# Kernel optimization log

Measured on AMD Instinct MI355X. Metric: run time of the kernel, lower is better.

## Reference

```python
import jax, jax.numpy as jnp
import numpy as np

N = 512
D_OBJ = 256
D_BOX = 128
D_IN = 2 * D_OBJ + D_BOX  # 640 = sum(input_dim)
HID = 256
D_OUT = 256               # sum(output_dim)
BN_EPS = 1e-5


def setup_inputs() -> dict:
    key = jax.random.key(0)
    ks = jax.random.split(key, 16)
    sc = lambda d: 1.0 / np.sqrt(d)
    inp = {
        "object_feats": jax.random.normal(ks[0], (N, D_OBJ), jnp.float32),
        "bboxes_embedding": jax.random.normal(ks[1], (N, N, D_BOX), jnp.float32),
        "mask": (jax.random.uniform(ks[2], (N, N)) > 0.3).astype(jnp.float32),
        # weight_mlp: Linear(D_IN->HID), LeakyReLU, BatchNorm1d(HID) [eval], Dropout [eval], Linear(HID->1)
        "w1": jax.random.normal(ks[3], (HID, D_IN), jnp.float32) * sc(D_IN),
        "b1": jnp.zeros((HID,), jnp.float32),
        "bn_gamma": jnp.ones((HID,), jnp.float32),
        "bn_beta": jnp.zeros((HID,), jnp.float32),
        "bn_mean": jnp.zeros((HID,), jnp.float32),
        "bn_var": jnp.ones((HID,), jnp.float32),
        "w2": jax.random.normal(ks[4], (1, HID), jnp.float32) * sc(HID),
        "b2": jnp.zeros((1,), jnp.float32),
        # conv: Linear(D_IN->HID), ReLU, Linear(HID->D_OUT)
        "cw1": jax.random.normal(ks[5], (HID, D_IN), jnp.float32) * sc(D_IN),
        "cb1": jnp.zeros((HID,), jnp.float32),
        "cw2": jax.random.normal(ks[6], (D_OUT, HID), jnp.float32) * sc(HID),
        "cb2": jnp.zeros((D_OUT,), jnp.float32),
    }
    return inp


def reference(object_feats, bboxes_embedding, mask, w1, b1, bn_gamma, bn_beta,
              bn_mean, bn_var, w2, b2, cw1, cb1, cw2, cb2):
    n = object_feats.shape[0]
    d = object_feats.shape[1]
    # all N^2 pairs (i, j) in row-major order: concat(feat_i, feat_j, bbox_ij)
    feats = jnp.concatenate([
        jnp.broadcast_to(object_feats[:, None, :], (n, n, d)),
        jnp.broadcast_to(object_feats[None, :, :], (n, n, d)),
        bboxes_embedding,
    ], axis=-1)                                        # [N, N, D_IN]

    # weight_mlp -> per-pair confidence scalar
    h = feats @ w1.T + b1                              # [N, N, HID]
    h = jnp.where(h > 0, h, 0.01 * h)                  # LeakyReLU(0.01)
    h = (h - bn_mean) * jax.lax.rsqrt(bn_var + BN_EPS) * bn_gamma + bn_beta
    conf = (h @ w2.T + b2)[..., 0]                     # [N, N]

    # row-wise softmax over j, masked renormalization
    conf = jax.nn.softmax(conf, axis=-1)
    conf = conf * mask
    conf = conf / (jnp.sum(conf, axis=-1, keepdims=True) + 1e-8)

    # conv MLP per pair, then weighted-sum reduce over neighbors j
    g = jax.nn.relu(feats @ cw1.T + cb1)               # [N, N, HID]
    out = g @ cw2.T + cb2                              # [N, N, D_OUT]
    new_feats = jnp.einsum('ij,ijd->id', conf, out)    # [N, D_OUT]
    return new_feats
```

## Files before the change

### kernel.cpp

```cpp
#include <hip/hip_runtime.h>
#include <hip/hip_bf16.h>

#define NN   512
#define DOBJ 256
#define DBOX 128
#define DIN  640
#define HID  256
#define DOUT 256

typedef __attribute__((ext_vector_type(8))) short  short8;
typedef __attribute__((ext_vector_type(4))) float  f32x4;

#define OFF_A    0u
#define OFF_B    131072u
#define OFF_CA   262144u
#define OFF_CB   393216u
#define OFF_WSV  524288u
#define OFF_S    524544u
#define OFF_CONF 525312u
#define OFF_G    787456u
#define OFF_WSWZ 918528u

__device__ __forceinline__ ushort bf16u(float x) {
    __hip_bfloat16 h = __float2bfloat16(x);
    union { __hip_bfloat16 b; ushort u; } c; c.b = h;
    return c.u;
}

__device__ __forceinline__ short8 cvt8(float4 a, float4 b) {
    short8 o;
    o[0] = (short)bf16u(a.x); o[1] = (short)bf16u(a.y);
    o[2] = (short)bf16u(a.z); o[3] = (short)bf16u(a.w);
    o[4] = (short)bf16u(b.x); o[5] = (short)bf16u(b.y);
    o[6] = (short)bf16u(b.z); o[7] = (short)bf16u(b.w);
    return o;
}

__global__ __launch_bounds__(256, 2) void k_pre_mfma(
    const float* __restrict__ obj, const float* __restrict__ w1,
    const float* __restrict__ cw1, const float* __restrict__ b1,
    const float* __restrict__ cb1,
    float* __restrict__ A, float* __restrict__ B,
    float* __restrict__ Ca, float* __restrict__ Cb)
{
    const int bx = blockIdx.x;
    const int i0 = blockIdx.y * 64;
    const int tid = threadIdx.x;
    const int w = tid >> 6, lane = tid & 63;
    const int lr = lane & 15, lg = lane >> 4;

    const float* src = (bx & 2) ? cw1 : w1;
    const int dof = (bx & 1) * DOBJ;

    f32x4 acc[4][4];
#pragma unroll
    for (int a = 0; a < 4; ++a)
#pragma unroll
        for (int b = 0; b < 4; ++b) acc[a][b] = (f32x4){0.f, 0.f, 0.f, 0.f};

#pragma unroll
    for (int ks = 0; ks < 8; ++ks) {
        short8 af[4], bf[4];
#pragma unroll
        for (int ms = 0; ms < 4; ++ms) {
            const float* ap = obj + (size_t)(i0 + ms * 16 + lr) * DOBJ + ks * 32 + lg * 8;
            af[ms] = cvt8(*(const float4*)ap, *(const float4*)(ap + 4));
        }
#pragma unroll
        for (int t = 0; t < 4; ++t) {
            const int kc = w * 64 + t * 16 + lr;
            const float* bp = src + (size_t)kc * DIN + dof + ks * 32 + lg * 8;
            bf[t] = cvt8(*(const float4*)bp, *(const float4*)(bp + 4));
        }
#pragma unroll
        for (int ms = 0; ms < 4; ++ms)
#pragma unroll
            for (int t = 0; t < 4; ++t)
                acc[ms][t] = __builtin_amdgcn_mfma_f32_16x16x32_bf16(
                    af[ms], bf[t], acc[ms][t], 0, 0, 0);
    }

    float* dst = (bx == 0) ? A : (bx == 1) ? B : (bx == 2) ? Ca : Cb;
    const float* bias = (bx == 0) ? b1 : (bx == 2) ? cb1 : nullptr;
    float bb[4];
#pragma unroll
    for (int t = 0; t < 4; ++t)
        bb[t] = bias ? bias[w * 64 + t * 16 + lr] : 0.f;

#pragma unroll
    for (int ms = 0; ms < 4; ++ms)
#pragma unroll
        for (int t = 0; t < 4; ++t)
#pragma unroll
            for (int r = 0; r < 4; ++r) {
                const int i = i0 + ms * 16 + lg * 4 + r;
                const int kc = w * 64 + t * 16 + lr;
                dst[(size_t)i * HID + kc] = acc[ms][t][r] + bb[t];
            }
}

__global__ void k_wsvec(const float* __restrict__ w2, const float* __restrict__ gamma,
                        const float* __restrict__ var, float* __restrict__ wsv)
{
    const int k = threadIdx.x;
    wsv[k] = w2[k] * gamma[k] * rsqrtf(var[k] + 1e-5f);
}

__global__ __launch_bounds__(128) void k_wprep(
    const float* __restrict__ w1, const float* __restrict__ cw1,
    ushort* __restrict__ wswz)
{
    const int k = blockIdx.x, mat = blockIdx.y, d = threadIdx.x;
    const float* src = mat ? cw1 : w1;
    const float v = src[(size_t)k * DIN + 2 * DOBJ + d];
    const int c = d >> 3;
    const int idx = k * 128 + (((c ^ (k & 7)) << 3)) + (d & 7);
    wswz[(size_t)mat * 32768 + idx] = bf16u(v);
}

template<int GACC>
__global__ __launch_bounds__(256, 2) void k_pair(
    const float* __restrict__ bbox, const ushort* __restrict__ wswz,
    const float* __restrict__ Arow,
    const float* __restrict__ Bcol,
    const float* __restrict__ aux,
    float* __restrict__ outp)
{
    const int i  = blockIdx.y;
    const int j0 = blockIdx.x * 64;
    const int tid = threadIdx.x;
    const int w = tid >> 6, lane = tid & 63;
    const int lr = lane & 15, lg = lane >> 4;

    __shared__ ushort wlds[32768];
    __shared__ float  red[4][64];
    __shared__ float  conf_s[64];

    {
        const uint4* g = (const uint4*)wswz;
        uint4* l = (uint4*)wlds;
#pragma unroll
        for (int n = 0; n < 16; ++n) l[n * 256 + tid] = g[n * 256 + tid];
    }
    if (GACC && tid < 64) conf_s[tid] = aux[(size_t)i * NN + j0 + tid];
    __syncthreads();

    float as_t[4], ws_t[4];
#pragma unroll
    for (int t = 0; t < 4; ++t) {
        const int kk = w * 64 + t * 16 + lr;
        as_t[t] = Arow[(size_t)i * HID + kk];
        ws_t[t] = GACC ? 0.f : aux[kk];
    }

    f32x4 acc[4][4];
#pragma unroll
    for (int a = 0; a < 4; ++a)
#pragma unroll
        for (int b = 0; b < 4; ++b) acc[a][b] = (f32x4){0.f, 0.f, 0.f, 0.f};

#pragma unroll
    for (int ks = 0; ks < 4; ++ks) {
        short8 bf[4];
#pragma unroll
        for (int t = 0; t < 4; ++t) {
            const int kk = w * 64 + t * 16 + lr;
            const int c  = (ks * 4 + lg) ^ (lr & 7);
            bf[t] = *(const short8*)&wlds[kk * 128 + (c << 3)];
        }
#pragma unroll
        for (int ms = 0; ms < 4; ++ms) {
            const float* ap = bbox +
                (((size_t)i * NN + j0 + ms * 16 + lr) * DBOX + ks * 32 + lg * 8);
            const float4 a0 = *(const float4*)ap;
            const float4 a1 = *(const float4*)(ap + 4);
            const short8 af = cvt8(a0, a1);
#pragma unroll
            for (int t = 0; t < 4; ++t)
                acc[ms][t] = __builtin_amdgcn_mfma_f32_16x16x32_bf16(
                    af, bf[t], acc[ms][t], 0, 0, 0);
        }
    }

    if (!GACC) {
        float pj[4][4];
#pragma unroll
        for (int a = 0; a < 4; ++a)
#pragma unroll
            for (int b = 0; b < 4; ++b) pj[a][b] = 0.f;
#pragma unroll
        for (int ms = 0; ms < 4; ++ms)
#pragma unroll
            for (int r = 0; r < 4; ++r) {
                const int j = j0 + ms * 16 + lg * 4 + r;
                const float* Bj = Bcol + (size_t)j * HID + w * 64 + lr;
#pragma unroll
                for (int t = 0; t < 4; ++t) {
                    float h = acc[ms][t][r] + as_t[t] + Bj[t * 16];
                    h = fmaxf(h, 0.01f * h);
                    pj[ms][r] = fmaf(h, ws_t[t], pj[ms][r]);
                }
            }
#pragma unroll
        for (int ms = 0; ms < 4; ++ms)
#pragma unroll
            for (int r = 0; r < 4; ++r) {
                float v = pj[ms][r];
                v += __shfl_xor(v, 1);  v += __shfl_xor(v, 2);
                v += __shfl_xor(v, 4);  v += __shfl_xor(v, 8);
                if (lr == 0) red[w][ms * 16 + lg * 4 + r] = v;
            }
        __syncthreads();
        if (tid < 64)
            outp[(size_t)i * NN + j0 + tid] =
                red[0][tid] + red[1][tid] + red[2][tid] + red[3][tid];
    } else {
        float cf[4][4];
#pragma unroll
        for (int ms = 0; ms < 4; ++ms)
#pragma unroll
            for (int r = 0; r < 4; ++r) cf[ms][r] = conf_s[ms * 16 + lg * 4 + r];
        float gk[4] = {0.f, 0.f, 0.f, 0.f};
#pragma unroll
        for (int ms = 0; ms < 4; ++ms)
#pragma unroll
            for (int r = 0; r < 4; ++r) {
                const int j = j0 + ms * 16 + lg * 4 + r;
                const float* Bj = Bcol + (size_t)j * HID + w * 64 + lr;
#pragma unroll
                for (int t = 0; t < 4; ++t) {
                    float h = acc[ms][t][r] + as_t[t] + Bj[t * 16];
                    h = fmaxf(h, 0.f);
                    gk[t] = fmaf(cf[ms][r], h, gk[t]);
                }
            }
#pragma unroll
        for (int t = 0; t < 4; ++t) {
            float v = gk[t];
            v += __shfl_xor(v, 16);
            v += __shfl_xor(v, 32);
            if (lg == 0)
                atomicAdd(&outp[(size_t)i * DOUT + w * 64 + t * 16 + lr], v);
        }
    }
}

__global__ __launch_bounds__(256) void k_softmax(
    const float* __restrict__ conf_raw, const float* __restrict__ mask,
    float* __restrict__ conf, float* __restrict__ s_out)
{
    const int i = blockIdx.x, tid = threadIdx.x;
    const int lane = tid & 63, w = tid >> 6;
    __shared__ float wred[3][4];

    const float r0 = conf_raw[(size_t)i * NN + tid];
    const float r1 = conf_raw[(size_t)i * NN + 256 + tid];
    const float mk0 = mask[(size_t)i * NN + tid];
    const float mk1 = mask[(size_t)i * NN + 256 + tid];

    float m = fmaxf(r0, r1);
#pragma unroll
    for (int off = 32; off; off >>= 1) m = fmaxf(m, __shfl_down(m, off));
    if (lane == 0) wred[0][w] = m;
    __syncthreads();
    const float M = fmaxf(fmaxf(wred[0][0], wred[0][1]), fmaxf(wred[0][2], wred[0][3]));

    const float e0 = __expf(r0 - M), e1 = __expf(r1 - M);
    float sa = e0 + e1;
    float sk = e0 * mk0 + e1 * mk1;
#pragma unroll
    for (int off = 32; off; off >>= 1) {
        sa += __shfl_down(sa, off);
        sk += __shfl_down(sk, off);
    }
    if (lane == 0) { wred[1][w] = sa; wred[2][w] = sk; }
    __syncthreads();
    const float SA = wred[1][0] + wred[1][1] + wred[1][2] + wred[1][3];
    const float SK = wred[2][0] + wred[2][1] + wred[2][2] + wred[2][3];
    const float dinv = 1.f / (SK + 1e-8f * SA);

    conf[(size_t)i * NN + tid]       = e0 * mk0 * dinv;
    conf[(size_t)i * NN + 256 + tid] = e1 * mk1 * dinv;
    if (tid == 0) s_out[i] = SK * dinv;
}

__global__ __launch_bounds__(256) void k_out(
    const float* __restrict__ G, const float* __restrict__ cw2,
    const float* __restrict__ cb2, const float* __restrict__ s_in,
    float* __restrict__ out)
{
    const int i = blockIdx.x, o = threadIdx.x;
    __shared__ float Gs[DOUT];
    Gs[o] = G[(size_t)i * DOUT + o];
    __syncthreads();
    const float* wr = cw2 + (size_t)o * HID;
    float acc = 0.f;
#pragma unroll 4
    for (int k = 0; k < HID; ++k) acc = fmaf(Gs[k], wr[k], acc);
    out[(size_t)i * DOUT + o] = acc + s_in[i] * cb2[o];
}

extern "C" void kernel_launch(void* const* d_in, const int* in_sizes, int n_in,
                              void* d_out, int out_size, void* d_ws, size_t ws_size,
                              hipStream_t stream)
{
    const float* obj  = (const float*)d_in[0];
    const float* bbox = (const float*)d_in[1];
    const float* mask = (const float*)d_in[2];
    const float* w1   = (const float*)d_in[3];
    const float* b1   = (const float*)d_in[4];
    const float* bn_g = (const float*)d_in[5];
    const float* bn_v = (const float*)d_in[8];
    const float* w2   = (const float*)d_in[9];
    const float* cw1  = (const float*)d_in[11];
    const float* cb1  = (const float*)d_in[12];
    const float* cw2  = (const float*)d_in[13];
    const float* cb2  = (const float*)d_in[14];

    float* ws   = (float*)d_ws;
    float* A    = ws + OFF_A;
    float* B    = ws + OFF_B;
    float* Ca   = ws + OFF_CA;
    float* Cb   = ws + OFF_CB;
    float* wsv  = ws + OFF_WSV;
    float* sbuf = ws + OFF_S;
    float* conf = ws + OFF_CONF;
    float* G    = ws + OFF_G;
    ushort* wswz = (ushort*)(ws + OFF_WSWZ);
    float* out  = (float*)d_out;

    k_pre_mfma<<<dim3(4, 8), 256, 0, stream>>>(obj, w1, cw1, b1, cb1, A, B, Ca, Cb);
    k_wsvec<<<1, 256, 0, stream>>>(w2, bn_g, bn_v, wsv);
    k_wprep<<<dim3(256, 2), 128, 0, stream>>>(w1, cw1, wswz);
    k_pair<0><<<dim3(8, NN), 256, 0, stream>>>(bbox, wswz, A, B, wsv, conf);
    k_softmax<<<NN, 256, 0, stream>>>(conf, mask, conf, sbuf);
    hipMemsetAsync(G, 0, (size_t)NN * DOUT * sizeof(float), stream);
    k_pair<1><<<dim3(8, NN), 256, 0, stream>>>(bbox, wswz + 32768, Ca, Cb, conf, G);
    k_out<<<NN, 256, 0, stream>>>(G, cw2, cb2, sbuf, out);
}
```

Measured before the change: 451.4 us.

## Fuse softmax into conf pair kernel and make G accumulation row-local

Restructures both pair kernels so one 512-thread block handles a whole row i, looping over four 128-column chunks. The row-wise softmax and mask renormalization are fused into the confidence kernel, and the G accumulation is reduced in shared memory instead of with global atomics. This removes the separate softmax launch, the memset, and the atomic traffic, and loads the LDS weights once per row instead of once per 64 columns. The cost is only 512 blocks with a serial j loop per block, which may lower parallelism and latency hiding.

```diff
diff --git a/kernel.cpp b/kernel.cpp
--- a/kernel.cpp
+++ b/kernel.cpp
@@ -118,170 +118,203 @@
     wswz[(size_t)mat * 32768 + idx] = bf16u(v);
 }
 
-template<int GACC>
-__global__ __launch_bounds__(256, 2) void k_pair(
+__global__ __launch_bounds__(512, 4) void k_conf_fused(
     const float* __restrict__ bbox, const ushort* __restrict__ wswz,
-    const float* __restrict__ Arow,
-    const float* __restrict__ Bcol,
-    const float* __restrict__ aux,
-    float* __restrict__ outp)
-{
-    const int i  = blockIdx.y;
-    const int j0 = blockIdx.x * 64;
+    const float* __restrict__ A_, const float* __restrict__ B_,
+    const float* __restrict__ wsv, const float* __restrict__ mask,
+    float* __restrict__ conf, float* __restrict__ s_out)
+{
+    const int i = blockIdx.x;
     const int tid = threadIdx.x;
-    const int w = tid >> 6, lane = tid & 63;
+    const int wv = tid >> 6, lane = tid & 63;
+    const int jw = wv >> 2, kw = wv & 3;
     const int lr = lane & 15, lg = lane >> 4;
 
     __shared__ ushort wlds[32768];
-    __shared__ float  red[4][64];
-    __shared__ float  conf_s[64];
+    __shared__ float  red[4][512];
+    __shared__ float  wred[3][8];
 
     {
         const uint4* g = (const uint4*)wswz;
         uint4* l = (uint4*)wlds;
 #pragma unroll
-        for (int n = 0; n < 16; ++n) l[n * 256 + tid] = g[n * 256 + tid];
-    }
-    if (GACC && tid < 64) conf_s[tid] = aux[(size_t)i * NN + j0 + tid];
+        for (int n = 0; n < 8; ++n) l[n * 512 + tid] = g[n * 512 + tid];
+    }
     __syncthreads();
 
     float as_t[4], ws_t[4];
 #pragma unroll
     for (int t = 0; t < 4; ++t) {
-        const int kk = w * 64 + t * 16 + lr;
-        as_t[t] = Arow[(size_t)i * HID + kk];
-        ws_t[t] = GACC ? 0.f : aux[kk];
-    }
-
-    f32x4 acc[4][4];
-#pragma unroll
-    for (int a = 0; a < 4; ++a)
-#pragma unroll
-        for (int b = 0; b < 4; ++b) acc[a][b] = (f32x4){0.f, 0.f, 0.f, 0.f};
-
-#pragma unroll
-    for (int ks = 0; ks < 4; ++ks) {
-        short8 bf[4];
-#pragma unroll
-        for (int t = 0; t < 4; ++t) {
-            const int kk = w * 64 + t * 16 + lr;
-            const int c  = (ks * 4 + lg) ^ (lr & 7);
-            bf[t] = *(const short8*)&wlds[kk * 128 + (c << 3)];
+        const int kk = kw * 64 + t * 16 + lr;
+        as_t[t] = A_[(size_t)i * HID + kk];
+        ws_t[t] = wsv[kk];
+    }
+
+    for (int it = 0; it < 4; ++it) {
+        const int j0 = it * 128 + jw * 64;
+
+        f32x4 acc[4][4];
+#pragma unroll
+        for (int a = 0; a < 4; ++a)
+#pragma unroll
+            for (int b = 0; b < 4; ++b) acc[a][b] = (f32x4){0.f, 0.f, 0.f, 0.f};
+
+#pragma unroll
+        for (int ks = 0; ks < 4; ++ks) {
+            short8 bf[4];
+#pragma unroll
+            for (int t = 0; t < 4; ++t) {
+                const int kk = kw * 64 + t * 16 + lr;
+                const int c  = (ks * 4 + lg) ^ (lr & 7);
+                bf[t] = *(const short8*)&wlds[kk * 128 + (c << 3)];
+            }
+#pragma unroll
+            for (int ms = 0; ms < 4; ++ms) {
+                const float* ap = bbox +
+                    (((size_t)i * NN + j0 + ms * 16 + lr) * DBOX + ks * 32 + lg * 8);
+                const short8 af = cvt8(*(const float4*)ap, *(const float4*)(ap + 4));
+#pragma unroll
+                for (int t = 0; t < 4; ++t)
+                    acc[ms][t] = __builtin_amdgcn_mfma_f32_16x16x32_bf16(
+                        af, bf[t], acc[ms][t], 0, 0, 0);
+            }
         }
-#pragma unroll
-        for (int ms = 0; ms < 4; ++ms) {
-            const float* ap = bbox +
-                (((size_t)i * NN + j0 + ms * 16 + lr) * DBOX + ks * 32 + lg * 8);
-            const float4 a0 = *(const float4*)ap;
-            const float4 a1 = *(const float4*)(ap + 4);
-            const short8 af = cvt8(a0, a1);
-#pragma unroll
-            for (int t = 0; t < 4; ++t)
-                acc[ms][t] = __builtin_amdgcn_mfma_f32_16x16x32_bf16(
-                    af, bf[t], acc[ms][t], 0, 0, 0);
-        }
-    }
-
-    if (!GACC) {
-        float pj[4][4];
-#pragma unroll
-        for (int a = 0; a < 4; ++a)
-#pragma unroll
-            for (int b = 0; b < 4; ++b) pj[a][b] = 0.f;
+
 #pragma unroll
         for (int ms = 0; ms < 4; ++ms)
 #pragma unroll
             for (int r = 0; r < 4; ++r) {
                 const int j = j0 + ms * 16 + lg * 4 + r;
-                const float* Bj = Bcol + (size_t)j * HID + w * 64 + lr;
+                const float* Bj = B_ + (size_t)j * HID + kw * 64 + lr;
+                float pj = 0.f;
 #pragma unroll
                 for (int t = 0; t < 4; ++t) {
                     float h = acc[ms][t][r] + as_t[t] + Bj[t * 16];
                     h = fmaxf(h, 0.01f * h);
-                    pj[ms][r] = fmaf(h, ws_t[t], pj[ms][r]);
+                    pj = fmaf(h, ws_t[t], pj);
                 }
-            }
-#pragma unroll
-        for (int ms = 0; ms < 4; ++ms)
-#pragma unroll
-            for (int r = 0; r < 4; ++r) {
-                float v = pj[ms][r];
-                v += __shfl_xor(v, 1);  v += __shfl_xor(v, 2);
-                v += __shfl_xor(v, 4);  v += __shfl_xor(v, 8);
-                if (lr == 0) red[w][ms * 16 + lg * 4 + r] = v;
-            }
-        __syncthreads();
-        if (tid < 64)
-            outp[(size_t)i * NN + j0 + tid] =
-                red[0][tid] + red[1][tid] + red[2][tid] + red[3][tid];
-    } else {
-        float cf[4][4];
-#pragma unroll
-        for (int ms = 0; ms < 4; ++ms)
-#pragma unroll
-            for (int r = 0; r < 4; ++r) cf[ms][r] = conf_s[ms * 16 + lg * 4 + r];
-        float gk[4] = {0.f, 0.f, 0.f, 0.f};
+                pj += __shfl_xor(pj, 1);  pj += __shfl_xor(pj, 2);
+                pj += __shfl_xor(pj, 4);  pj += __shfl_xor(pj, 8);
+                if (lr == 0) red[kw][j] = pj;
+            }
+    }
+    __syncthreads();
+
+    const float r0 = red[0][tid] + red[1][tid] + red[2][tid] + red[3][tid];
+    const float mk = mask[(size_t)i * NN + tid];
+
+    float m = r0;
+#pragma unroll
+    for (int off = 32; off; off >>= 1) m = fmaxf(m, __shfl_xor(m, off));
+    if (lane == 0) wred[0][wv] = m;
+    __syncthreads();
+    float M = wred[0][0];
+#pragma unroll
+    for (int u = 1; u < 8; ++u) M = fmaxf(M, wred[0][u]);
+
+    const float e = __expf(r0 - M);
+    float sa = e, sk = e * mk;
+#pragma unroll
+    for (int off = 32; off; off >>= 1) {
+        sa += __shfl_xor(sa, off);
+        sk += __shfl_xor(sk, off);
+    }
+    if (lane == 0) { wred[1][wv] = sa; wred[2][wv] = sk; }
+    __syncthreads();
+    float SA = 0.f, SK = 0.f;
+#pragma unroll
+    for (int u = 0; u < 8; ++u) { SA += wred[1][u]; SK += wred[2][u]; }
+    const float dinv = 1.f / (SK + 1e-8f * SA);
+
+    conf[(size_t)i * NN + tid] = e * mk * dinv;
+    if (tid == 0) s_out[i] = SK * dinv;
+}
+
+__global__ __launch_bounds__(512, 4) void k_gacc_fused(
+    const float* __restrict__ bbox, const ushort* __restrict__ wswz,
+    const float* __restrict__ Ca_, const float* __restrict__ Cb_,
+    const float* __restrict__ conf, float* __restrict__ G)
+{
+    const int i = blockIdx.x;
+    const int tid = threadIdx.x;
+    const int wv = tid >> 6, lane = tid & 63;
+    const int jw = wv >> 2, kw = wv & 3;
+    const int lr = lane & 15, lg = lane >> 4;
+
+    __shared__ ushort wlds[32768];
+    __shared__ float  conf_s[512];
+    __shared__ float  gred[2][256];
+
+    {
+        const uint4* g = (const uint4*)wswz;
+        uint4* l = (uint4*)wlds;
+#pragma unroll
+        for (int n = 0; n < 8; ++n) l[n * 512 + tid] = g[n * 512 + tid];
+    }
+    conf_s[tid] = conf[(size_t)i * NN + tid];
+    __syncthreads();
+
+    float as_t[4];
+#pragma unroll
+    for (int t = 0; t < 4; ++t)
+        as_t[t] = Ca_[(size_t)i * HID + kw * 64 + t * 16 + lr];
+
+    float gk[4] = {0.f, 0.f, 0.f, 0.f};
+
+    for (int it = 0; it < 4; ++it) {
+        const int j0 = it * 128 + jw * 64;
+
+        f32x4 acc[4][4];
+#pragma unroll
+        for (int a = 0; a < 4; ++a)
+#pragma unroll
+            for (int b = 0; b < 4; ++b) acc[a][b] = (f32x4){0.f, 0.f, 0.f, 0.f};
+
+#pragma unroll
+        for (int ks = 0; ks < 4; ++ks) {
+            short8 bf[4];
+#pragma unroll
+            for (int t = 0; t < 4; ++t) {
+                const int kk = kw * 64 + t * 16 + lr;
+                const int c  = (ks * 4 + lg) ^ (lr & 7);
+                bf[t] = *(const short8*)&wlds[kk * 128 + (c << 3)];
+            }
+#pragma unroll
+            for (int ms = 0; ms < 4; ++ms) {
+                const float* ap = bbox +
+                    (((size_t)i * NN + j0 + ms * 16 + lr) * DBOX + ks * 32 + lg * 8);
+                const short8 af = cvt8(*(const float4*)ap, *(const float4*)(ap + 4));
+#pragma unroll
+                for (int t = 0; t < 4; ++t)
+                    acc[ms][t] = __builtin_amdgcn_mfma_f32_16x16x32_bf16(
+                        af, bf[t], acc[ms][t], 0, 0, 0);
+            }
+        }
+
 #pragma unroll
         for (int ms = 0; ms < 4; ++ms)
 #pragma unroll
             for (int r = 0; r < 4; ++r) {
                 const int j = j0 + ms * 16 + lg * 4 + r;
-                const float* Bj = Bcol + (size_t)j * HID + w * 64 + lr;
+                const float cf = conf_s[j];
+                const float* Bj = Cb_ + (size_t)j * HID + kw * 64 + lr;
 #pragma unroll
                 for (int t = 0; t < 4; ++t) {
                     float h = acc[ms][t][r] + as_t[t] + Bj[t * 16];
-                    h = fmaxf(h, 0.f);
-                    gk[t] = fmaf(cf[ms][r], h, gk[t]);
+                    gk[t] = fmaf(cf, fmaxf(h, 0.f), gk[t]);
                 }
             }
-#pragma unroll
-        for (int t = 0; t < 4; ++t) {
-            float v = gk[t];
-            v += __shfl_xor(v, 16);
-            v += __shfl_xor(v, 32);
-            if (lg == 0)
-                atomicAdd(&outp[(size_t)i * DOUT + w * 64 + t * 16 + lr], v);
-        }
-    }
-}
-
-__global__ __launch_bounds__(256) void k_softmax(
-    const float* __restrict__ conf_raw, const float* __restrict__ mask,
-    float* __restrict__ conf, float* __restrict__ s_out)
-{
-    const int i = blockIdx.x, tid = threadIdx.x;
-    const int lane = tid & 63, w = tid >> 6;
-    __shared__ float wred[3][4];
-
-    const float r0 = conf_raw[(size_t)i * NN + tid];
-    const float r1 = conf_raw[(size_t)i * NN + 256 + tid];
-    const float mk0 = mask[(size_t)i * NN + tid];
-    const float mk1 = mask[(size_t)i * NN + 256 + tid];
-
-    float m = fmaxf(r0, r1);
-#pragma unroll
-    for (int off = 32; off; off >>= 1) m = fmaxf(m, __shfl_down(m, off));
-    if (lane == 0) wred[0][w] = m;
-    __syncthreads();
-    const float M = fmaxf(fmaxf(wred[0][0], wred[0][1]), fmaxf(wred[0][2], wred[0][3]));
-
-    const float e0 = __expf(r0 - M), e1 = __expf(r1 - M);
-    float sa = e0 + e1;
-    float sk = e0 * mk0 + e1 * mk1;
-#pragma unroll
-    for (int off = 32; off; off >>= 1) {
-        sa += __shfl_down(sa, off);
-        sk += __shfl_down(sk, off);
-    }
-    if (lane == 0) { wred[1][w] = sa; wred[2][w] = sk; }
-    __syncthreads();
-    const float SA = wred[1][0] + wred[1][1] + wred[1][2] + wred[1][3];
-    const float SK = wred[2][0] + wred[2][1] + wred[2][2] + wred[2][3];
-    const float dinv = 1.f / (SK + 1e-8f * SA);
-
-    conf[(size_t)i * NN + tid]       = e0 * mk0 * dinv;
-    conf[(size_t)i * NN + 256 + tid] = e1 * mk1 * dinv;
-    if (tid == 0) s_out[i] = SK * dinv;
+    }
+
+#pragma unroll
+    for (int t = 0; t < 4; ++t) {
+        float v = gk[t];
+        v += __shfl_xor(v, 16);
+        v += __shfl_xor(v, 32);
+        if (lg == 0) gred[jw][kw * 64 + t * 16 + lr] = v;
+    }
+    __syncthreads();
+    if (tid < 256) G[(size_t)i * DOUT + tid] = gred[0][tid] + gred[1][tid];
 }
 
 __global__ __launch_bounds__(256) void k_out(
@@ -332,9 +365,7 @@
     k_pre_mfma<<<dim3(4, 8), 256, 0, stream>>>(obj, w1, cw1, b1, cb1, A, B, Ca, Cb);
     k_wsvec<<<1, 256, 0, stream>>>(w2, bn_g, bn_v, wsv);
     k_wprep<<<dim3(256, 2), 128, 0, stream>>>(w1, cw1, wswz);
-    k_pair<0><<<dim3(8, NN), 256, 0, stream>>>(bbox, wswz, A, B, wsv, conf);
-    k_softmax<<<NN, 256, 0, stream>>>(conf, mask, conf, sbuf);
-    hipMemsetAsync(G, 0, (size_t)NN * DOUT * sizeof(float), stream);
-    k_pair<1><<<dim3(8, NN), 256, 0, stream>>>(bbox, wswz + 32768, Ca, Cb, conf, G);
+    k_conf_fused<<<NN, 512, 0, stream>>>(bbox, wswz, A, B, wsv, mask, conf, sbuf);
+    k_gacc_fused<<<NN, 512, 0, stream>>>(bbox, wswz + 32768, Ca, Cb, conf, G);
     k_out<<<NN, 256, 0, stream>>>(G, cw2, cb2, sbuf, out);
 }
```

Result: slower. 546.3 us (+21.0%).

## Hold bbox weights in registers and loop over several rows per block

Applied to the files above, without the earlier changes.

Each pair kernel now loads its bbox-slice weights straight from global memory into registers once per block and reuses them across GI=8 rows i. This replaces the per-block LDS staging of the full pre-swizzled weight tile and cuts the grid size eightfold. The small prep kernels (wsvec, wprep) and the memset are folded into the pair and softmax kernels, which removes launches. In exchange, register pressure rises (16 short8 weight fragments per thread), each block works through its rows serially, and occupancy may drop.

```diff
diff --git a/kernel.cpp b/kernel.cpp
--- a/kernel.cpp
+++ b/kernel.cpp
@@ -7,6 +7,7 @@
 #define DIN  640
 #define HID  256
 #define DOUT 256
+#define GI   8
 
 typedef __attribute__((ext_vector_type(8))) short  short8;
 typedef __attribute__((ext_vector_type(4))) float  f32x4;
@@ -15,11 +16,9 @@
 #define OFF_B    131072u
 #define OFF_CA   262144u
 #define OFF_CB   393216u
-#define OFF_WSV  524288u
 #define OFF_S    524544u
 #define OFF_CONF 525312u
 #define OFF_G    787456u
-#define OFF_WSWZ 918528u
 
 __device__ __forceinline__ ushort bf16u(float x) {
     __hip_bfloat16 h = __float2bfloat16(x);
@@ -99,139 +98,188 @@
             }
 }
 
-__global__ void k_wsvec(const float* __restrict__ w2, const float* __restrict__ gamma,
-                        const float* __restrict__ var, float* __restrict__ wsv)
-{
-    const int k = threadIdx.x;
-    wsv[k] = w2[k] * gamma[k] * rsqrtf(var[k] + 1e-5f);
-}
-
-__global__ __launch_bounds__(128) void k_wprep(
-    const float* __restrict__ w1, const float* __restrict__ cw1,
-    ushort* __restrict__ wswz)
-{
-    const int k = blockIdx.x, mat = blockIdx.y, d = threadIdx.x;
-    const float* src = mat ? cw1 : w1;
-    const float v = src[(size_t)k * DIN + 2 * DOBJ + d];
-    const int c = d >> 3;
-    const int idx = k * 128 + (((c ^ (k & 7)) << 3)) + (d & 7);
-    wswz[(size_t)mat * 32768 + idx] = bf16u(v);
-}
-
-template<int GACC>
-__global__ __launch_bounds__(256, 2) void k_pair(
-    const float* __restrict__ bbox, const ushort* __restrict__ wswz,
-    const float* __restrict__ Arow,
-    const float* __restrict__ Bcol,
-    const float* __restrict__ aux,
-    float* __restrict__ outp)
-{
-    const int i  = blockIdx.y;
+__global__ __launch_bounds__(256, 2) void k_conf(
+    const float* __restrict__ bbox, const float* __restrict__ w1,
+    const float* __restrict__ A_, const float* __restrict__ B_,
+    const float* __restrict__ w2, const float* __restrict__ bn_g,
+    const float* __restrict__ bn_v, float* __restrict__ conf_raw)
+{
     const int j0 = blockIdx.x * 64;
+    const int i0 = blockIdx.y * GI;
     const int tid = threadIdx.x;
     const int w = tid >> 6, lane = tid & 63;
     const int lr = lane & 15, lg = lane >> 4;
 
-    __shared__ ushort wlds[32768];
-    __shared__ float  red[4][64];
-    __shared__ float  conf_s[64];
-
-    {
-        const uint4* g = (const uint4*)wswz;
-        uint4* l = (uint4*)wlds;
-#pragma unroll
-        for (int n = 0; n < 16; ++n) l[n * 256 + tid] = g[n * 256 + tid];
-    }
-    if (GACC && tid < 64) conf_s[tid] = aux[(size_t)i * NN + j0 + tid];
-    __syncthreads();
-
-    float as_t[4], ws_t[4];
+    __shared__ float red[2][4][64];
+
+    short8 bf[4][4];
+    float ws_t[4];
 #pragma unroll
     for (int t = 0; t < 4; ++t) {
         const int kk = w * 64 + t * 16 + lr;
-        as_t[t] = Arow[(size_t)i * HID + kk];
-        ws_t[t] = GACC ? 0.f : aux[kk];
-    }
-
-    f32x4 acc[4][4];
-#pragma unroll
-    for (int a = 0; a < 4; ++a)
-#pragma unroll
-        for (int b = 0; b < 4; ++b) acc[a][b] = (f32x4){0.f, 0.f, 0.f, 0.f};
-
-#pragma unroll
-    for (int ks = 0; ks < 4; ++ks) {
-        short8 bf[4];
-#pragma unroll
-        for (int t = 0; t < 4; ++t) {
-            const int kk = w * 64 + t * 16 + lr;
-            const int c  = (ks * 4 + lg) ^ (lr & 7);
-            bf[t] = *(const short8*)&wlds[kk * 128 + (c << 3)];
-        }
-#pragma unroll
-        for (int ms = 0; ms < 4; ++ms) {
-            const float* ap = bbox +
-                (((size_t)i * NN + j0 + ms * 16 + lr) * DBOX + ks * 32 + lg * 8);
-            const float4 a0 = *(const float4*)ap;
-            const float4 a1 = *(const float4*)(ap + 4);
-            const short8 af = cvt8(a0, a1);
-#pragma unroll
-            for (int t = 0; t < 4; ++t)
-                acc[ms][t] = __builtin_amdgcn_mfma_f32_16x16x32_bf16(
-                    af, bf[t], acc[ms][t], 0, 0, 0);
-        }
-    }
-
-    if (!GACC) {
-        float pj[4][4];
+        ws_t[t] = w2[kk] * bn_g[kk] * rsqrtf(bn_v[kk] + 1e-5f);
+#pragma unroll
+        for (int ks = 0; ks < 4; ++ks) {
+            const float* bp = w1 + (size_t)kk * DIN + 2 * DOBJ + ks * 32 + lg * 8;
+            bf[t][ks] = cvt8(*(const float4*)bp, *(const float4*)(bp + 4));
+        }
+    }
+
+    for (int g = 0; g < GI; ++g) {
+        const int i = i0 + g;
+        const int p = g & 1;
+
+        float as_t[4];
+#pragma unroll
+        for (int t = 0; t < 4; ++t)
+            as_t[t] = A_[(size_t)i * HID + w * 64 + t * 16 + lr];
+
+        f32x4 acc[4][4];
 #pragma unroll
         for (int a = 0; a < 4; ++a)
 #pragma unroll
-            for (int b = 0; b < 4; ++b) pj[a][b] = 0.f;
+            for (int b = 0; b < 4; ++b) acc[a][b] = (f32x4){0.f, 0.f, 0.f, 0.f};
+
+#pragma unroll
+        for (int ks = 0; ks < 4; ++ks)
+#pragma unroll
+            for (int ms = 0; ms < 4; ++ms) {
+                const float* ap = bbox +
+                    (((size_t)i * NN + j0 + ms * 16 + lr) * DBOX + ks * 32 + lg * 8);
+                const short8 af = cvt8(*(const float4*)ap, *(const float4*)(ap + 4));
+#pragma unroll
+                for (int t = 0; t < 4; ++t)
+                    acc[ms][t] = __builtin_amdgcn_mfma_f32_16x16x32_bf16(
+                        af, bf[t][ks], acc[ms][t], 0, 0, 0);
+            }
+
 #pragma unroll
         for (int ms = 0; ms < 4; ++ms)
 #pragma unroll
             for (int r = 0; r < 4; ++r) {
                 const int j = j0 + ms * 16 + lg * 4 + r;
-                const float* Bj = Bcol + (size_t)j * HID + w * 64 + lr;
+                const float* Bj = B_ + (size_t)j * HID + w * 64 + lr;
+                float pj = 0.f;
 #pragma unroll
                 for (int t = 0; t < 4; ++t) {
                     float h = acc[ms][t][r] + as_t[t] + Bj[t * 16];
                     h = fmaxf(h, 0.01f * h);
-                    pj[ms][r] = fmaf(h, ws_t[t], pj[ms][r]);
+                    pj = fmaf(h, ws_t[t], pj);
                 }
-            }
-#pragma unroll
-        for (int ms = 0; ms < 4; ++ms)
-#pragma unroll
-            for (int r = 0; r < 4; ++r) {
-                float v = pj[ms][r];
-                v += __shfl_xor(v, 1);  v += __shfl_xor(v, 2);
-                v += __shfl_xor(v, 4);  v += __shfl_xor(v, 8);
-                if (lr == 0) red[w][ms * 16 + lg * 4 + r] = v;
+                pj += __shfl_xor(pj, 1);  pj += __shfl_xor(pj, 2);
+                pj += __shfl_xor(pj, 4);  pj += __shfl_xor(pj, 8);
+                if (lr == 0) red[p][w][ms * 16 + lg * 4 + r] = pj;
             }
         __syncthreads();
         if (tid < 64)
-            outp[(size_t)i * NN + j0 + tid] =
-                red[0][tid] + red[1][tid] + red[2][tid] + red[3][tid];
-    } else {
-        float cf[4][4];
+            conf_raw[(size_t)i * NN + j0 + tid] =
+                red[p][0][tid] + red[p][1][tid] + red[p][2][tid] + red[p][3][tid];
+    }
+}
+
+__global__ __launch_bounds__(256) void k_softmax(
+    const float* __restrict__ conf_raw, const float* __restrict__ mask,
+    float* __restrict__ conf, float* __restrict__ s_out, float* __restrict__ G)
+{
+    const int i = blockIdx.x, tid = threadIdx.x;
+    const int lane = tid & 63, w = tid >> 6;
+    __shared__ float wred[3][4];
+
+    G[(size_t)i * DOUT + tid] = 0.f;
+
+    const float r0 = conf_raw[(size_t)i * NN + tid];
+    const float r1 = conf_raw[(size_t)i * NN + 256 + tid];
+    const float mk0 = mask[(size_t)i * NN + tid];
+    const float mk1 = mask[(size_t)i * NN + 256 + tid];
+
+    float m = fmaxf(r0, r1);
+#pragma unroll
+    for (int off = 32; off; off >>= 1) m = fmaxf(m, __shfl_down(m, off));
+    if (lane == 0) wred[0][w] = m;
+    __syncthreads();
+    const float M = fmaxf(fmaxf(wred[0][0], wred[0][1]), fmaxf(wred[0][2], wred[0][3]));
+
+    const float e0 = __expf(r0 - M), e1 = __expf(r1 - M);
+    float sa = e0 + e1;
+    float sk = e0 * mk0 + e1 * mk1;
+#pragma unroll
+    for (int off = 32; off; off >>= 1) {
+        sa += __shfl_down(sa, off);
+        sk += __shfl_down(sk, off);
+    }
+    if (lane == 0) { wred[1][w] = sa; wred[2][w] = sk; }
+    __syncthreads();
+    const float SA = wred[1][0] + wred[1][1] + wred[1][2] + wred[1][3];
+    const float SK = wred[2][0] + wred[2][1] + wred[2][2] + wred[2][3];
+    const float dinv = 1.f / (SK + 1e-8f * SA);
+
+    conf[(size_t)i * NN + tid]       = e0 * mk0 * dinv;
+    conf[(size_t)i * NN + 256 + tid] = e1 * mk1 * dinv;
+    if (tid == 0) s_out[i] = SK * dinv;
+}
+
+__global__ __launch_bounds__(256, 2) void k_gacc(
+    const float* __restrict__ bbox, const float* __restrict__ cw1,
+    const float* __restrict__ Ca_, const float* __restrict__ Cb_,
+    const float* __restrict__ conf, float* __restrict__ G)
+{
+    const int j0 = blockIdx.x * 64;
+    const int i0 = blockIdx.y * GI;
+    const int tid = threadIdx.x;
+    const int w = tid >> 6, lane = tid & 63;
+    const int lr = lane & 15, lg = lane >> 4;
+
+    short8 bf[4][4];
+#pragma unroll
+    for (int t = 0; t < 4; ++t) {
+        const int kk = w * 64 + t * 16 + lr;
+#pragma unroll
+        for (int ks = 0; ks < 4; ++ks) {
+            const float* bp = cw1 + (size_t)kk * DIN + 2 * DOBJ + ks * 32 + lg * 8;
+            bf[t][ks] = cvt8(*(const float4*)bp, *(const float4*)(bp + 4));
+        }
+    }
+
+    for (int g = 0; g < GI; ++g) {
+        const int i = i0 + g;
+
+        float as_t[4];
+#pragma unroll
+        for (int t = 0; t < 4; ++t)
+            as_t[t] = Ca_[(size_t)i * HID + w * 64 + t * 16 + lr];
+
+        f32x4 acc[4][4];
+#pragma unroll
+        for (int a = 0; a < 4; ++a)
+#pragma unroll
+            for (int b = 0; b < 4; ++b) acc[a][b] = (f32x4){0.f, 0.f, 0.f, 0.f};
+
+#pragma unroll
+        for (int ks = 0; ks < 4; ++ks)
+#pragma unroll
+            for (int ms = 0; ms < 4; ++ms) {
+                const float* ap = bbox +
+                    (((size_t)i * NN + j0 + ms * 16 + lr) * DBOX + ks * 32 + lg * 8);
+                const short8 af = cvt8(*(const float4*)ap, *(const float4*)(ap + 4));
+#pragma unroll
+                for (int t = 0; t < 4; ++t)
+                    acc[ms][t] = __builtin_amdgcn_mfma_f32_16x16x32_bf16(
+                        af, bf[t][ks], acc[ms][t], 0, 0, 0);
+            }
+
+        const float* cfrow = conf + (size_t)i * NN + j0;
+        float gk[4] = {0.f, 0.f, 0.f, 0.f};
 #pragma unroll
         for (int ms = 0; ms < 4; ++ms)
 #pragma unroll
-            for (int r = 0; r < 4; ++r) cf[ms][r] = conf_s[ms * 16 + lg * 4 + r];
-        float gk[4] = {0.f, 0.f, 0.f, 0.f};
-#pragma unroll
-        for (int ms = 0; ms < 4; ++ms)
-#pragma unroll
             for (int r = 0; r < 4; ++r) {
-                const int j = j0 + ms * 16 + lg * 4 + r;
-                const float* Bj = Bcol + (size_t)j * HID + w * 64 + lr;
+                const int jL = ms * 16 + lg * 4 + r;
+                const float cf = cfrow[jL];
+                const float* Bj = Cb_ + (size_t)(j0 + jL) * HID + w * 64 + lr;
 #pragma unroll
                 for (int t = 0; t < 4; ++t) {
                     float h = acc[ms][t][r] + as_t[t] + Bj[t * 16];
-                    h = fmaxf(h, 0.f);
-                    gk[t] = fmaf(cf[ms][r], h, gk[t]);
+                    gk[t] = fmaf(cf, fmaxf(h, 0.f), gk[t]);
                 }
             }
 #pragma unroll
@@ -240,48 +288,9 @@
             v += __shfl_xor(v, 16);
             v += __shfl_xor(v, 32);
             if (lg == 0)
-                atomicAdd(&outp[(size_t)i * DOUT + w * 64 + t * 16 + lr], v);
-        }
-    }
-}
-
-__global__ __launch_bounds__(256) void k_softmax(
-    const float* __restrict__ conf_raw, const float* __restrict__ mask,
-    float* __restrict__ conf, float* __restrict__ s_out)
-{
-    const int i = blockIdx.x, tid = threadIdx.x;
-    const int lane = tid & 63, w = tid >> 6;
-    __shared__ float wred[3][4];
-
-    const float r0 = conf_raw[(size_t)i * NN + tid];
-    const float r1 = conf_raw[(size_t)i * NN + 256 + tid];
-    const float mk0 = mask[(size_t)i * NN + tid];
-    const float mk1 = mask[(size_t)i * NN + 256 + tid];
-
-    float m = fmaxf(r0, r1);
-#pragma unroll
-    for (int off = 32; off; off >>= 1) m = fmaxf(m, __shfl_down(m, off));
-    if (lane == 0) wred[0][w] = m;
-    __syncthreads();
-    const float M = fmaxf(fmaxf(wred[0][0], wred[0][1]), fmaxf(wred[0][2], wred[0][3]));
-
-    const float e0 = __expf(r0 - M), e1 = __expf(r1 - M);
-    float sa = e0 + e1;
-    float sk = e0 * mk0 + e1 * mk1;
-#pragma unroll
-    for (int off = 32; off; off >>= 1) {
-        sa += __shfl_down(sa, off);
-        sk += __shfl_down(sk, off);
-    }
-    if (lane == 0) { wred[1][w] = sa; wred[2][w] = sk; }
-    __syncthreads();
-    const float SA = wred[1][0] + wred[1][1] + wred[1][2] + wred[1][3];
-    const float SK = wred[2][0] + wred[2][1] + wred[2][2] + wred[2][3];
-    const float dinv = 1.f / (SK + 1e-8f * SA);
-
-    conf[(size_t)i * NN + tid]       = e0 * mk0 * dinv;
-    conf[(size_t)i * NN + 256 + tid] = e1 * mk1 * dinv;
-    if (tid == 0) s_out[i] = SK * dinv;
+                atomicAdd(&G[(size_t)i * DOUT + w * 64 + t * 16 + lr], v);
+        }
+    }
 }
 
 __global__ __launch_bounds__(256) void k_out(
@@ -322,19 +331,14 @@
     float* B    = ws + OFF_B;
     float* Ca   = ws + OFF_CA;
     float* Cb   = ws + OFF_CB;
-    float* wsv  = ws + OFF_WSV;
     float* sbuf = ws + OFF_S;
     float* conf = ws + OFF_CONF;
     float* G    = ws + OFF_G;
-    ushort* wswz = (ushort*)(ws + OFF_WSWZ);
     float* out  = (float*)d_out;
 
     k_pre_mfma<<<dim3(4, 8), 256, 0, stream>>>(obj, w1, cw1, b1, cb1, A, B, Ca, Cb);
-    k_wsvec<<<1, 256, 0, stream>>>(w2, bn_g, bn_v, wsv);
-    k_wprep<<<dim3(256, 2), 128, 0, stream>>>(w1, cw1, wswz);
-    k_pair<0><<<dim3(8, NN), 256, 0, stream>>>(bbox, wswz, A, B, wsv, conf);
-    k_softmax<<<NN, 256, 0, stream>>>(conf, mask, conf, sbuf);
-    hipMemsetAsync(G, 0, (size_t)NN * DOUT * sizeof(float), stream);
-    k_pair<1><<<dim3(8, NN), 256, 0, stream>>>(bbox, wswz + 32768, Ca, Cb, conf, G);
+    k_conf<<<dim3(8, NN / GI), 256, 0, stream>>>(bbox, w1, A, B, w2, bn_g, bn_v, conf);
+    k_softmax<<<NN, 256, 0, stream>>>(conf, mask, conf, sbuf, G);
+    k_gacc<<<dim3(8, NN / GI), 256, 0, stream>>>(bbox, cw1, Ca, Cb, conf, G);
     k_out<<<NN, 256, 0, stream>>>(G, cw2, cb2, sbuf, out);
 }
```

Measured after the change: 408.0 us. -9.6%, faster.
